# Performance work log

Hardware: AMD Instinct MI355X
Metric: run time of the kernel (lower is better)

The kernel has to match this reference:

```python
import jax, jax.numpy as jnp
import numpy as np
import math

N_HEADS = 64
N_KV_HEADS = 8
HEAD_DIM = 128
DIM = 8192
SEQLEN = 2048
KVLEN = 2048
BSZ = 1


def setup_inputs() -> dict:
    key = jax.random.key(0)
    k1, k2, k3, k4, k5 = jax.random.split(key, 5)
    xq = jax.random.normal(k1, (SEQLEN, N_HEADS, BSZ, HEAD_DIM), dtype=jnp.float32)
    keys = jax.random.normal(k2, (BSZ, N_KV_HEADS, KVLEN, HEAD_DIM), dtype=jnp.float32)
    values = jax.random.normal(k3, (BSZ, N_KV_HEADS, KVLEN, HEAD_DIM), dtype=jnp.float32)
    attn_mask = jax.random.normal(k4, (SEQLEN, 1, 1, KVLEN), dtype=jnp.float32)
    wo_w = jax.random.normal(k5, (DIM, DIM), dtype=jnp.float32) * (1.0 / math.sqrt(DIM))
    return {"xq": xq, "keys": keys, "values": values, "attn_mask": attn_mask, "wo_w": wo_w}


def reference(xq, keys, values, attn_mask, wo_w):
    n_rep = N_HEADS // N_KV_HEADS
    bsz = xq.shape[2]
    seqlen = xq.shape[0]
    # repeat_kv: expand kv heads to n_heads (torch expand+reshape == jnp.repeat on head axis)
    k = jnp.repeat(keys, n_rep, axis=1)    # (b, n_heads, kv, d)
    v = jnp.repeat(values, n_rep, axis=1)  # (b, n_heads, kv, d)
    q = jnp.transpose(xq, (2, 1, 0, 3))    # (b, n_heads, s, d)
    mask = jnp.transpose(attn_mask, (2, 1, 0, 3))  # (b_or_1, h_or_1, s, kv)
    scores = jnp.einsum('bhsd,bhtd->bhst', q, k) / math.sqrt(HEAD_DIM)
    scores = scores + mask
    probs = jax.nn.softmax(scores.astype(jnp.float32), axis=-1).astype(q.dtype)
    out = jnp.einsum('bhst,bhtd->bhsd', probs, v)  # (b, h, s, d)
    out = jnp.transpose(out, (0, 2, 1, 3)).reshape(bsz, seqlen, -1)  # (b, s, h*d)
    return out @ wo_w.T  # Linear wo, no bias
```

## Files before the change

kernel.cpp:

```cpp
#include <hip/hip_runtime.h>
#include <hip/hip_bf16.h>
#include <stdint.h>


typedef __bf16 bf16;
typedef __attribute__((ext_vector_type(8))) __bf16 bf16x8;
typedef __attribute__((ext_vector_type(4))) __bf16 bf16x4;
typedef __attribute__((ext_vector_type(4))) float f32x4;
typedef __attribute__((ext_vector_type(16))) float f32x16;
typedef __attribute__((ext_vector_type(4))) unsigned int u32x4;

#define N_HEADS 64
#define N_KVH   8
#define HDIM    128
#define SEQ     2048
#define KVL     2048
#define DIM     8192

__device__ __forceinline__ void gload16(const void* g, void* l) {
  __builtin_amdgcn_global_load_lds((const __attribute__((address_space(1))) void*)g,
                                   (__attribute__((address_space(3))) void*)l,
                                   16, 0, 0);
}

__device__ __forceinline__ unsigned pack2(float lo, float hi) {
  union { bf16 h; unsigned short u; } a, b;
  a.h = (bf16)lo; b.h = (bf16)hi;
  return ((unsigned)b.u << 16) | (unsigned)a.u;
}

__device__ __forceinline__ void exch(unsigned a, unsigned b, bool hi, unsigned& r0, unsigned& r1) {
  unsigned sa = (unsigned)__shfl_xor((int)a, 32);
  unsigned sb = (unsigned)__shfl_xor((int)b, 32);
  r0 = hi ? sb : a;
  r1 = hi ? b  : sa;
}

__device__ __forceinline__ void buildfrags(const float (&p)[16], bool hi, bf16x8& f0, bf16x8& f1) {
  unsigned pk0 = pack2(p[0],  p[1]),  pk1 = pack2(p[2],  p[3]);
  unsigned pk2 = pack2(p[4],  p[5]),  pk3 = pack2(p[6],  p[7]);
  unsigned pk4 = pack2(p[8],  p[9]),  pk5 = pack2(p[10], p[11]);
  unsigned pk6 = pack2(p[12], p[13]), pk7 = pack2(p[14], p[15]);
  unsigned a0, a1, b0, b1, c0, c1, d0, d1;
  exch(pk0, pk2, hi, a0, a1);
  exch(pk1, pk3, hi, b0, b1);
  exch(pk4, pk6, hi, c0, c1);
  exch(pk5, pk7, hi, d0, d1);
  u32x4 w0 = { a0, b0, a1, b1 };
  u32x4 w1 = { c0, d0, c1, d1 };
  f0 = __builtin_bit_cast(bf16x8, w0);
  f1 = __builtin_bit_cast(bf16x8, w1);
}

__global__ void cvt_f32_bf16(const float* __restrict__ in, bf16* __restrict__ out, int n4) {
  int i = blockIdx.x * blockDim.x + threadIdx.x;
  int stride = gridDim.x * blockDim.x;
  for (; i < n4; i += stride) {
    float4 v = ((const float4*)in)[i];
    bf16x4 o = { (bf16)v.x, (bf16)v.y, (bf16)v.z, (bf16)v.w };
    *(bf16x4*)(out + (long)i * 4) = o;
  }
}

__global__ void cvt_vT_kernel(const float* __restrict__ v, bf16* __restrict__ vT) {
  __shared__ bf16 tile[64][132];
  const int tid = threadIdx.x;
  const int kh = blockIdx.x >> 5;
  const int t0 = (blockIdx.x & 31) << 6;
  const float* src = v + ((long)kh * KVL + t0) * HDIM;
#pragma unroll
  for (int it = 0; it < 8; ++it) {
    int q = it * 256 + tid;
    int r = q >> 5;
    int c4 = (q & 31) << 2;
    float4 val = *(const float4*)(src + (long)r * HDIM + c4);
    bf16x4 o = { (bf16)val.x, (bf16)val.y, (bf16)val.z, (bf16)val.w };
    *(bf16x4*)&tile[r][c4] = o;
  }
  __syncthreads();
  const int t = tid & 63;
  const int dbase = tid >> 6;
#pragma unroll
  for (int it = 0; it < 32; ++it) {
    int d = it * 4 + dbase;
    vT[((long)kh * HDIM + d) * KVL + t0 + t] = tile[t][d];
  }
}

__global__ __launch_bounds__(512, 2) void attn_kernel(
    const bf16* __restrict__ qB, const bf16* __restrict__ kB,
    const bf16* __restrict__ vT, const float* __restrict__ mask,
    bf16* __restrict__ attnB)
{
  __shared__ __align__(16) char lds[65536];

  const int tid  = threadIdx.x;
  const int lane = tid & 63;
  const int w    = tid >> 6;
  const bool hi  = (lane >> 5) != 0;
  const int ihi  = lane >> 5;
  const int l31  = lane & 31;

  const int bid = blockIdx.x;
  const int h   = bid >> 3;
  const int q0b = (bid & 7) << 8;
  const int kh  = h >> 3;

#pragma unroll
  for (int rnd = 0; rnd < 8; ++rnd) {
    int row = rnd * 32 + w * 4 + (lane >> 4);
    int cg  = (lane & 15) ^ (row & 15);
    const bf16* g = qB + (((long)(q0b + row) * N_HEADS + h) << 7) + (cg << 3);
    gload16(g, lds + rnd * 8192 + w * 1024);
  }
  __syncthreads();

  bf16x8 qf[8];
  {
    int qrow = (w << 5) + l31;
    const char* qr = lds + qrow * 256;
#pragma unroll
    for (int s = 0; s < 8; ++s)
      qf[s] = *(const bf16x8*)(qr + ((((s << 1) | ihi) ^ (qrow & 15)) << 4));
  }
  __syncthreads();

  {
#pragma unroll
    for (int rnd = 0; rnd < 2; ++rnd) {
      int row = rnd * 32 + w * 4 + (lane >> 4);
      int cg  = (lane & 15) ^ (row & 15);
      const bf16* g = kB + (((long)(kh * KVL + row)) << 7) + (cg << 3);
      gload16(g, lds + rnd * 8192 + w * 1024);
    }
#pragma unroll
    for (int rnd = 0; rnd < 2; ++rnd) {
      int vr = rnd * 32 + w * 4 + (lane >> 4);
      int gg = (lane & 15) ^ (vr & 15);
      int dsrc = (vr << 1) | (gg >> 3);
      const bf16* gp = vT + ((long)(kh * HDIM + dsrc) * KVL) + ((gg & 7) << 3);
      gload16(gp, lds + 32768 + rnd * 8192 + w * 1024);
    }
  }
  __syncthreads();

  const float scale = 0.08838834764831845f;
  const float* mrow = mask + (size_t)(q0b + (w << 5) + l31) * KVL + (ihi << 2);

  f32x16 acc[4];
#pragma unroll
  for (int dt = 0; dt < 4; ++dt) acc[dt] = {};
  float m_run = -1e30f, l_run = 0.f;

  for (int kt = 0; kt < KVL / 64; ++kt) {
    const int cur = kt & 1;
    const int kv0 = kt << 6;

    if (kt < KVL / 64 - 1) {
      const int kv0n = kv0 + 64;
#pragma unroll
      for (int rnd = 0; rnd < 2; ++rnd) {
        int row = rnd * 32 + w * 4 + (lane >> 4);
        int cg  = (lane & 15) ^ (row & 15);
        const bf16* g = kB + (((long)(kh * KVL + kv0n + row)) << 7) + (cg << 3);
        gload16(g, lds + (cur ^ 1) * 16384 + rnd * 8192 + w * 1024);
      }
#pragma unroll
      for (int rnd = 0; rnd < 2; ++rnd) {
        int vr = rnd * 32 + w * 4 + (lane >> 4);
        int gg = (lane & 15) ^ (vr & 15);
        int dsrc = (vr << 1) | (gg >> 3);
        const bf16* gp = vT + ((long)(kh * HDIM + dsrc) * KVL) + kv0n + ((gg & 7) << 3);
        gload16(gp, lds + 32768 + (cur ^ 1) * 16384 + rnd * 8192 + w * 1024);
      }
    }

    const float* mrt = mrow + kv0;
    f32x4 mk0[4], mk1[4];
#pragma unroll
    for (int rq = 0; rq < 4; ++rq) {
      mk0[rq] = *(const f32x4*)(mrt + (rq << 3));
      mk1[rq] = *(const f32x4*)(mrt + 32 + (rq << 3));
    }

    const char* kb = lds + cur * 16384;
    f32x16 s0 = {}, s1 = {};
    const int kr0 = l31, kr1 = 32 + l31;
    __builtin_amdgcn_s_setprio(1);
#pragma unroll
    for (int s = 0; s < 8; ++s) {
      bf16x8 kf0 = *(const bf16x8*)(kb + kr0 * 256 + ((((s << 1) | ihi) ^ (kr0 & 15)) << 4));
      s0 = __builtin_amdgcn_mfma_f32_32x32x16_bf16(kf0, qf[s], s0, 0, 0, 0);
      bf16x8 kf1 = *(const bf16x8*)(kb + kr1 * 256 + ((((s << 1) | ihi) ^ (kr1 & 15)) << 4));
      s1 = __builtin_amdgcn_mfma_f32_32x32x16_bf16(kf1, qf[s], s1, 0, 0, 0);
    }
    __builtin_amdgcn_s_setprio(0);

    float p0[16], p1[16];
#pragma unroll
    for (int rq = 0; rq < 4; ++rq) {
#pragma unroll
      for (int j = 0; j < 4; ++j) {
        p0[rq * 4 + j] = s0[rq * 4 + j] * scale + mk0[rq][j];
        p1[rq * 4 + j] = s1[rq * 4 + j] * scale + mk1[rq][j];
      }
    }

    float q00 = fmaxf(fmaxf(p0[0],  p0[1]),  fmaxf(p0[2],  p0[3]));
    float q01 = fmaxf(fmaxf(p0[4],  p0[5]),  fmaxf(p0[6],  p0[7]));
    float q02 = fmaxf(fmaxf(p0[8],  p0[9]),  fmaxf(p0[10], p0[11]));
    float q03 = fmaxf(fmaxf(p0[12], p0[13]), fmaxf(p0[14], p0[15]));
    float q10 = fmaxf(fmaxf(p1[0],  p1[1]),  fmaxf(p1[2],  p1[3]));
    float q11 = fmaxf(fmaxf(p1[4],  p1[5]),  fmaxf(p1[6],  p1[7]));
    float q12 = fmaxf(fmaxf(p1[8],  p1[9]),  fmaxf(p1[10], p1[11]));
    float q13 = fmaxf(fmaxf(p1[12], p1[13]), fmaxf(p1[14], p1[15]));
    float mx = fmaxf(fmaxf(fmaxf(q00, q01), fmaxf(q02, q03)),
                     fmaxf(fmaxf(q10, q11), fmaxf(q12, q13)));
    mx = fmaxf(mx, __shfl_xor(mx, 32));
    if (!__all((int)(mx - m_run <= 8.0f))) {
      float nm = fmaxf(m_run, mx);
      float al = __expf(m_run - nm);
      m_run = nm;
      l_run *= al;
#pragma unroll
      for (int dt = 0; dt < 4; ++dt) acc[dt] *= al;
    }
    float ps = 0.f;
#pragma unroll
    for (int i = 0; i < 16; ++i) { p0[i] = __expf(p0[i] - m_run); ps += p0[i]; }
#pragma unroll
    for (int i = 0; i < 16; ++i) { p1[i] = __expf(p1[i] - m_run); ps += p1[i]; }
    ps += __shfl_xor(ps, 32);
    l_run += ps;

    bf16x8 pfrag[4];
    buildfrags(p0, hi, pfrag[0], pfrag[1]);
    buildfrags(p1, hi, pfrag[2], pfrag[3]);

    const char* vb = lds + 32768 + cur * 16384;
    const int par8 = (l31 & 1) << 3;
    __builtin_amdgcn_s_setprio(1);
#pragma unroll
    for (int dt = 0; dt < 4; ++dt) {
      const int vrow = (dt << 4) + (l31 >> 1);
      const char* vrp = vb + vrow * 256;
#pragma unroll
      for (int ks = 0; ks < 4; ++ks) {
        int c16 = par8 | (ks << 1) | ihi;
        bf16x8 vf = *(const bf16x8*)(vrp + ((c16 ^ (vrow & 15)) << 4));
        acc[dt] = __builtin_amdgcn_mfma_f32_32x32x16_bf16(vf, pfrag[ks], acc[dt], 0, 0, 0);
      }
    }
    __builtin_amdgcn_s_setprio(0);
    __syncthreads();
  }

  const float linv = 1.0f / l_run;
  char* ep = lds + (w << 13);
#pragma unroll
  for (int dt = 0; dt < 4; ++dt) {
#pragma unroll
    for (int r = 0; r < 16; ++r) {
      int d = (dt << 5) + (r & 3) + ((r >> 2) << 3) + (ihi << 2);
      int byte = l31 * 256 + (((d >> 3) ^ (l31 & 15)) << 4) + ((d & 7) << 1);
      *(bf16*)(ep + byte) = (bf16)(acc[dt][r] * linv);
    }
  }
  __syncthreads();
  const size_t obase = (size_t)(q0b + (w << 5)) * DIM + h * HDIM;
#pragma unroll
  for (int i = 0; i < 8; ++i) {
    int row = (i << 2) + (lane >> 4);
    int cp  = lane & 15;
    int c   = cp ^ (row & 15);
    bf16x8 ov = *(const bf16x8*)(ep + row * 256 + (cp << 4));
    *(bf16x8*)(attnB + obase + (size_t)row * DIM + (c << 3)) = ov;
  }
}

__global__ __launch_bounds__(512, 2) void gemm_bt(
    const bf16* __restrict__ A, const bf16* __restrict__ B, float* __restrict__ C)
{
  __shared__ __align__(16) char lds[131072];
  const int tid  = threadIdx.x;
  const int lane = tid & 63;
  const int w    = tid >> 6;
  const int wm   = w >> 2;
  const int wn   = w & 3;

  const int bid = blockIdx.x;
  const int m0  = (bid >> 5) << 8;
  const int n0  = (((bid & 7) << 2) | ((bid >> 3) & 3)) << 8;

  const int srow = tid >> 2;
  const int skey = (srow >> 1) & 3;
  const int sch  = (tid & 3) ^ skey;
  const bf16* gA0 = A + (long)(m0 + srow) * DIM + (sch << 3);
  const bf16* gA1 = gA0 + (long)128 * DIM;
  const bf16* gB0 = B + (long)(n0 + srow) * DIM + (sch << 3);
  const bf16* gB1 = gB0 + (long)128 * DIM;

  f32x4 acc[8][4];
#pragma unroll
  for (int i = 0; i < 8; ++i)
#pragma unroll
    for (int j = 0; j < 4; ++j) acc[i][j] = { 0.f, 0.f, 0.f, 0.f };

  auto STAGE = [&](int kt) {
    const long ko = (long)kt << 5;
    char* s = lds + (kt & 3) * 32768 + (w << 10);
    gload16(gA0 + ko, s);
    gload16(gA1 + ko, s + 8192);
    gload16(gB0 + ko, s + 16384);
    gload16(gB1 + ko, s + 24576);
  };

  const int g = lane >> 4;
  auto COMPUTE = [&](int slot) {
    const char* ab = lds + slot * 32768;
    const char* bb = ab + 16384;
    bf16x8 af[8], bfr[4];
#pragma unroll
    for (int i = 0; i < 8; ++i) {
      int m = (wm << 7) + (i << 4) + (lane & 15);
      af[i] = *(const bf16x8*)(ab + m * 64 + ((g ^ ((m >> 1) & 3)) << 4));
    }
#pragma unroll
    for (int j = 0; j < 4; ++j) {
      int n = (wn << 6) + (j << 4) + (lane & 15);
      bfr[j] = *(const bf16x8*)(bb + n * 64 + ((g ^ ((n >> 1) & 3)) << 4));
    }
    __builtin_amdgcn_s_setprio(1);
#pragma unroll
    for (int i = 0; i < 8; ++i)
#pragma unroll
      for (int j = 0; j < 4; ++j)
        acc[i][j] = __builtin_amdgcn_mfma_f32_16x16x32_bf16(af[i], bfr[j], acc[i][j], 0, 0, 0);
    __builtin_amdgcn_s_setprio(0);
  };

  STAGE(0);
  STAGE(1);
  STAGE(2);

#pragma unroll 4
  for (int t = 0; t < 252; ++t) {
    asm volatile("s_waitcnt vmcnt(8)" ::: "memory");
    __builtin_amdgcn_s_barrier();
    STAGE(t + 3);
    COMPUTE(t & 3);
  }
  asm volatile("s_waitcnt vmcnt(8)" ::: "memory");
  __builtin_amdgcn_s_barrier();
  STAGE(255);
  COMPUTE(0);
  asm volatile("s_waitcnt vmcnt(8)" ::: "memory");
  __builtin_amdgcn_s_barrier();
  COMPUTE(1);
  asm volatile("s_waitcnt vmcnt(4)" ::: "memory");
  __builtin_amdgcn_s_barrier();
  COMPUTE(2);
  asm volatile("s_waitcnt vmcnt(0)" ::: "memory");
  __builtin_amdgcn_s_barrier();
  COMPUTE(3);

#pragma unroll
  for (int i = 0; i < 8; ++i) {
#pragma unroll
    for (int rr = 0; rr < 4; ++rr) {
      float* cp = C + (long)(m0 + (wm << 7) + (i << 4) + ((lane >> 4) << 2) + rr) * DIM
                    + n0 + (wn << 6) + (lane & 15);
#pragma unroll
      for (int j = 0; j < 4; ++j)
        cp[j * 16] = acc[i][j][rr];
    }
  }
}

extern "C" void kernel_launch(void* const* d_in, const int* in_sizes, int n_in,
                              void* d_out, int out_size, void* d_ws, size_t ws_size,
                              hipStream_t stream) {
  const float* xq     = (const float*)d_in[0];
  const float* keys   = (const float*)d_in[1];
  const float* values = (const float*)d_in[2];
  const float* mask   = (const float*)d_in[3];
  const float* wo     = (const float*)d_in[4];
  float* out = (float*)d_out;
  char* ws = (char*)d_ws;

  bf16* woB = (bf16*)ws;
  bf16* qB  = (bf16*)(ws + 134217728ull);
  bf16* kB  = (bf16*)(ws + 134217728ull + 33554432ull);
  bf16* vT  = (bf16*)(ws + 134217728ull + 37748736ull);
  bf16* aB  = (bf16*)(ws + 134217728ull + 41943040ull);

  cvt_f32_bf16<<<dim3(2048), dim3(256), 0, stream>>>(wo, woB, 16777216);
  cvt_f32_bf16<<<dim3(1024), dim3(256), 0, stream>>>(xq, qB, 4194304);
  cvt_f32_bf16<<<dim3(256),  dim3(256), 0, stream>>>(keys, kB, 524288);
  cvt_vT_kernel<<<dim3(256), dim3(256), 0, stream>>>(values, vT);
  attn_kernel<<<dim3(512),   dim3(512), 0, stream>>>(qB, kB, vT, mask, aB);
  gemm_bt<<<dim3(256),       dim3(512), 0, stream>>>(aB, woB, out);
}
```

Baseline: 553.8 us.

## Fold softmax scale into Q conversion, use permlane32 swap, restructure GEMM staging

Result: no change. 552.1 us (-0.3%).

```diff
diff --git a/kernel.cpp b/kernel.cpp
--- a/kernel.cpp
+++ b/kernel.cpp
@@ -29,35 +29,35 @@
   return ((unsigned)b.u << 16) | (unsigned)a.u;
 }
 
-__device__ __forceinline__ void exch(unsigned a, unsigned b, bool hi, unsigned& r0, unsigned& r1) {
-  unsigned sa = (unsigned)__shfl_xor((int)a, 32);
-  unsigned sb = (unsigned)__shfl_xor((int)b, 32);
-  r0 = hi ? sb : a;
-  r1 = hi ? b  : sa;
-}
-
-__device__ __forceinline__ void buildfrags(const float (&p)[16], bool hi, bf16x8& f0, bf16x8& f1) {
+__device__ __forceinline__ void exch(unsigned a, unsigned b, unsigned& r0, unsigned& r1) {
+  asm("v_permlane32_swap_b32 %0, %1" : "+v"(a), "+v"(b));
+  r0 = a; r1 = b;
+}
+
+__device__ __forceinline__ void buildfrags(const float (&p)[16], bf16x8& f0, bf16x8& f1) {
   unsigned pk0 = pack2(p[0],  p[1]),  pk1 = pack2(p[2],  p[3]);
   unsigned pk2 = pack2(p[4],  p[5]),  pk3 = pack2(p[6],  p[7]);
   unsigned pk4 = pack2(p[8],  p[9]),  pk5 = pack2(p[10], p[11]);
   unsigned pk6 = pack2(p[12], p[13]), pk7 = pack2(p[14], p[15]);
   unsigned a0, a1, b0, b1, c0, c1, d0, d1;
-  exch(pk0, pk2, hi, a0, a1);
-  exch(pk1, pk3, hi, b0, b1);
-  exch(pk4, pk6, hi, c0, c1);
-  exch(pk5, pk7, hi, d0, d1);
+  exch(pk0, pk2, a0, a1);
+  exch(pk1, pk3, b0, b1);
+  exch(pk4, pk6, c0, c1);
+  exch(pk5, pk7, d0, d1);
   u32x4 w0 = { a0, b0, a1, b1 };
   u32x4 w1 = { c0, d0, c1, d1 };
   f0 = __builtin_bit_cast(bf16x8, w0);
   f1 = __builtin_bit_cast(bf16x8, w1);
 }
 
-__global__ void cvt_f32_bf16(const float* __restrict__ in, bf16* __restrict__ out, int n4) {
+__global__ void cvt_f32_bf16(const float* __restrict__ in, bf16* __restrict__ out,
+                             int n4, float scale) {
   int i = blockIdx.x * blockDim.x + threadIdx.x;
   int stride = gridDim.x * blockDim.x;
   for (; i < n4; i += stride) {
     float4 v = ((const float4*)in)[i];
-    bf16x4 o = { (bf16)v.x, (bf16)v.y, (bf16)v.z, (bf16)v.w };
+    bf16x4 o = { (bf16)(v.x * scale), (bf16)(v.y * scale),
+                 (bf16)(v.z * scale), (bf16)(v.w * scale) };
     *(bf16x4*)(out + (long)i * 4) = o;
   }
 }
@@ -97,7 +97,6 @@
   const int tid  = threadIdx.x;
   const int lane = tid & 63;
   const int w    = tid >> 6;
-  const bool hi  = (lane >> 5) != 0;
   const int ihi  = lane >> 5;
   const int l31  = lane & 31;
 
@@ -144,7 +143,6 @@
   }
   __syncthreads();
 
-  const float scale = 0.08838834764831845f;
   const float* mrow = mask + (size_t)(q0b + (w << 5) + l31) * KVL + (ihi << 2);
 
   f32x16 acc[4];
@@ -201,8 +199,8 @@
     for (int rq = 0; rq < 4; ++rq) {
 #pragma unroll
       for (int j = 0; j < 4; ++j) {
-        p0[rq * 4 + j] = s0[rq * 4 + j] * scale + mk0[rq][j];
-        p1[rq * 4 + j] = s1[rq * 4 + j] * scale + mk1[rq][j];
+        p0[rq * 4 + j] = s0[rq * 4 + j] + mk0[rq][j];
+        p1[rq * 4 + j] = s1[rq * 4 + j] + mk1[rq][j];
       }
     }
 
@@ -234,8 +232,8 @@
     l_run += ps;
 
     bf16x8 pfrag[4];
-    buildfrags(p0, hi, pfrag[0], pfrag[1]);
-    buildfrags(p1, hi, pfrag[2], pfrag[3]);
+    buildfrags(p0, pfrag[0], pfrag[1]);
+    buildfrags(p1, pfrag[2], pfrag[3]);
 
     const char* vb = lds + 32768 + cur * 16384;
     const int par8 = (l31 & 1) << 3;
@@ -292,13 +290,11 @@
   const int m0  = (bid >> 5) << 8;
   const int n0  = (((bid & 7) << 2) | ((bid >> 3) & 3)) << 8;
 
-  const int srow = tid >> 2;
-  const int skey = (srow >> 1) & 3;
-  const int sch  = (tid & 3) ^ skey;
+  const int srow = tid >> 3;
+  const int sch  = (tid & 7) ^ (srow & 7);
   const bf16* gA0 = A + (long)(m0 + srow) * DIM + (sch << 3);
-  const bf16* gA1 = gA0 + (long)128 * DIM;
   const bf16* gB0 = B + (long)(n0 + srow) * DIM + (sch << 3);
-  const bf16* gB1 = gB0 + (long)128 * DIM;
+  const long rstep = (long)64 * DIM;
 
   f32x4 acc[8][4];
 #pragma unroll
@@ -307,69 +303,78 @@
     for (int j = 0; j < 4; ++j) acc[i][j] = { 0.f, 0.f, 0.f, 0.f };
 
   auto STAGE = [&](int kt) {
-    const long ko = (long)kt << 5;
-    char* s = lds + (kt & 3) * 32768 + (w << 10);
-    gload16(gA0 + ko, s);
-    gload16(gA1 + ko, s + 8192);
-    gload16(gB0 + ko, s + 16384);
-    gload16(gB1 + ko, s + 24576);
+    const long ko = (long)kt << 6;
+    char* s = lds + (kt & 1) * 65536 + tid * 16;
+#pragma unroll
+    for (int l = 0; l < 4; ++l)
+      gload16(gA0 + l * rstep + ko, s + l * 8192);
+#pragma unroll
+    for (int l = 0; l < 4; ++l)
+      gload16(gB0 + l * rstep + ko, s + 32768 + l * 8192);
   };
 
   const int g = lane >> 4;
-  auto COMPUTE = [&](int slot) {
-    const char* ab = lds + slot * 32768;
-    const char* bb = ab + 16384;
-    bf16x8 af[8], bfr[4];
-#pragma unroll
-    for (int i = 0; i < 8; ++i) {
-      int m = (wm << 7) + (i << 4) + (lane & 15);
-      af[i] = *(const bf16x8*)(ab + m * 64 + ((g ^ ((m >> 1) & 3)) << 4));
-    }
+  const int l15 = lane & 15;
+  auto COMPUTE = [&](int buf) {
+    const char* ab = lds + buf * 65536;
+    const char* bb = ab + 32768;
+    bf16x8 bfr[4][2];
 #pragma unroll
     for (int j = 0; j < 4; ++j) {
-      int n = (wn << 6) + (j << 4) + (lane & 15);
-      bfr[j] = *(const bf16x8*)(bb + n * 64 + ((g ^ ((n >> 1) & 3)) << 4));
-    }
-    __builtin_amdgcn_s_setprio(1);
-#pragma unroll
-    for (int i = 0; i < 8; ++i)
-#pragma unroll
-      for (int j = 0; j < 4; ++j)
-        acc[i][j] = __builtin_amdgcn_mfma_f32_16x16x32_bf16(af[i], bfr[j], acc[i][j], 0, 0, 0);
-    __builtin_amdgcn_s_setprio(0);
+      int n = (wn << 6) + (j << 4) + l15;
+      const char* nr = bb + n * 128;
+#pragma unroll
+      for (int ks = 0; ks < 2; ++ks)
+        bfr[j][ks] = *(const bf16x8*)(nr + ((((ks << 2) | g) ^ (n & 7)) << 4));
+    }
+#pragma unroll
+    for (int p = 0; p < 4; ++p) {
+      bf16x8 af[2][2];
+#pragma unroll
+      for (int e = 0; e < 2; ++e) {
+        int m = (wm << 7) + (((p << 1) | e) << 4) + l15;
+        const char* mr = ab + m * 128;
+#pragma unroll
+        for (int ks = 0; ks < 2; ++ks)
+          af[e][ks] = *(const bf16x8*)(mr + ((((ks << 2) | g) ^ (m & 7)) << 4));
+      }
+      __builtin_amdgcn_s_setprio(1);
+#pragma unroll
+      for (int e = 0; e < 2; ++e)
+#pragma unroll
+        for (int j = 0; j < 4; ++j)
+#pragma unroll
+          for (int ks = 0; ks < 2; ++ks)
+            acc[(p << 1) | e][j] =
+              __builtin_amdgcn_mfma_f32_16x16x32_bf16(af[e][ks], bfr[j][ks],
+                                                      acc[(p << 1) | e][j], 0, 0, 0);
+      __builtin_amdgcn_s_setprio(0);
+    }
   };
 
   STAGE(0);
   STAGE(1);
-  STAGE(2);
-
-#pragma unroll 4
-  for (int t = 0; t < 252; ++t) {
+
+  for (int t = 0; t < 126; ++t) {
     asm volatile("s_waitcnt vmcnt(8)" ::: "memory");
     __builtin_amdgcn_s_barrier();
-    STAGE(t + 3);
-    COMPUTE(t & 3);
+    COMPUTE(t & 1);
+    __builtin_amdgcn_s_barrier();
+    STAGE(t + 2);
   }
   asm volatile("s_waitcnt vmcnt(8)" ::: "memory");
   __builtin_amdgcn_s_barrier();
-  STAGE(255);
   COMPUTE(0);
-  asm volatile("s_waitcnt vmcnt(8)" ::: "memory");
+  asm volatile("s_waitcnt vmcnt(0)" ::: "memory");
   __builtin_amdgcn_s_barrier();
   COMPUTE(1);
-  asm volatile("s_waitcnt vmcnt(4)" ::: "memory");
-  __builtin_amdgcn_s_barrier();
-  COMPUTE(2);
-  asm volatile("s_waitcnt vmcnt(0)" ::: "memory");
-  __builtin_amdgcn_s_barrier();
-  COMPUTE(3);
 
 #pragma unroll
   for (int i = 0; i < 8; ++i) {
 #pragma unroll
     for (int rr = 0; rr < 4; ++rr) {
       float* cp = C + (long)(m0 + (wm << 7) + (i << 4) + ((lane >> 4) << 2) + rr) * DIM
-                    + n0 + (wn << 6) + (lane & 15);
+                    + n0 + (wn << 6) + l15;
 #pragma unroll
       for (int j = 0; j < 4; ++j)
         cp[j * 16] = acc[i][j][rr];
@@ -394,9 +399,9 @@
   bf16* vT  = (bf16*)(ws + 134217728ull + 37748736ull);
   bf16* aB  = (bf16*)(ws + 134217728ull + 41943040ull);
 
-  cvt_f32_bf16<<<dim3(2048), dim3(256), 0, stream>>>(wo, woB, 16777216);
-  cvt_f32_bf16<<<dim3(1024), dim3(256), 0, stream>>>(xq, qB, 4194304);
-  cvt_f32_bf16<<<dim3(256),  dim3(256), 0, stream>>>(keys, kB, 524288);
+  cvt_f32_bf16<<<dim3(2048), dim3(256), 0, stream>>>(wo, woB, 16777216, 1.0f);
+  cvt_f32_bf16<<<dim3(1024), dim3(256), 0, stream>>>(xq, qB, 4194304, 0.08838834764831845f);
+  cvt_f32_bf16<<<dim3(256),  dim3(256), 0, stream>>>(keys, kB, 524288, 1.0f);
   cvt_vT_kernel<<<dim3(256), dim3(256), 0, stream>>>(values, vT);
   attn_kernel<<<dim3(512),   dim3(512), 0, stream>>>(qB, kB, vT, mask, aB);
   gemm_bt<<<dim3(256),       dim3(512), 0, stream>>>(aB, woB, out);
```
